# Kernel tuning notes

Measured on AMD Instinct MI355X. Metric: run time of the kernel, lower is better.

The kernel has to match this reference:

```python
import jax, jax.numpy as jnp
import numpy as np

D = 1024
B, T = 4, 2048


def setup_inputs() -> dict:
    key = jax.random.key(0)
    ks = jax.random.split(key, 7)
    s = 0.02
    return {
        "x": jax.random.normal(ks[0], (B, T, D), dtype=jnp.float32),
        "W_in": s * jax.random.normal(ks[1], (2 * D, D), dtype=jnp.float32),
        "b_in": jnp.zeros((2 * D,), dtype=jnp.float32),
        "W_s": s * jax.random.normal(ks[2], (D, D), dtype=jnp.float32),
        "b_s": jnp.zeros((D,), dtype=jnp.float32),
        "W_o": s * jax.random.normal(ks[3], (D, D), dtype=jnp.float32),
        "b_o": jnp.zeros((D,), dtype=jnp.float32),
    }


def _scan_combine(c1, c2):
    # h_t = a_t * h_{t-1} + b_t  -> associative composition of affine maps
    a1, b1 = c1
    a2, b2 = c2
    return a2 * a1, a2 * b1 + b2


def reference(x, W_in, b_in, W_s, b_s, W_o, b_o):
    # Batched projections over all timesteps (h-independent)
    gv = jnp.einsum("btd,ed->bte", x, W_in) + b_in          # [B,T,2D]
    gate = jax.nn.sigmoid(gv[..., :D])                        # [B,T,D]
    val = gv[..., D:]                                         # [B,T,D]
    sv = jnp.tanh(jnp.einsum("btd,ed->bte", val, W_s) + b_s)  # [B,T,D]
    # Linear recurrence h_t = (1-gate_t)*h_{t-1} + gate_t*sv_t, h_0 = 0
    a = 1.0 - gate
    b = gate * sv
    _, h = jax.lax.associative_scan(_scan_combine, (a, b), axis=1)  # h: [B,T,D]
    out = jnp.einsum("btd,ed->bte", h, W_o) + b_o
    return x + out
```

## Files before the change

### kernel.cpp

```cpp
#include <hip/hip_runtime.h>
#include <hip/hip_bf16.h>
#include <cmath>

#define B_DIM 4
#define T_DIM 2048
#define D_DIM 1024
#define M_DIM 8192
#define KP    2048

#define NCH   64
#define CHL   32

using bf16 = __hip_bfloat16;
typedef __attribute__((ext_vector_type(8))) short frag8;
typedef __attribute__((ext_vector_type(4))) float f32x4;

#define XS_OFF   0L
#define WIN_OFF  33554432L
#define WSS_OFF  37748736L
#define WOS_OFF  39845888L
#define GATE_OFF 41943040L
#define VS_OFF   75497472L
#define AF_OFF   92274688L
#define BF_OFF   125829120L
#define ACH_OFF  159383552L
#define BCH_OFF  160432128L

__global__ void split_kernel(const float* __restrict__ src, bf16* __restrict__ dst, long total4) {
    long i4 = (long)blockIdx.x * blockDim.x + threadIdx.x;
    if (i4 >= total4) return;
    long i = i4 * 4;
    const float4 v = *(const float4*)&src[i];
    long r = i >> 10;
    int  c = (int)(i & 1023);
    ushort hi[4], lo[4];
    const float vv[4] = {v.x, v.y, v.z, v.w};
#pragma unroll
    for (int j = 0; j < 4; ++j) {
        bf16 h = __float2bfloat16(vv[j]);
        hi[j] = *(ushort*)&h;
        bf16 l2 = __float2bfloat16(vv[j] - __bfloat162float(h));
        lo[j] = *(ushort*)&l2;
    }
    *(ushort4*)&dst[r * KP + c]        = make_ushort4(hi[0], hi[1], hi[2], hi[3]);
    *(ushort4*)&dst[r * KP + c + 1024] = make_ushort4(lo[0], lo[1], lo[2], lo[3]);
}

__global__ void wconv_kernel(const float* __restrict__ Win, const float* __restrict__ Wsm,
                             const float* __restrict__ Wo,
                             bf16* __restrict__ Wins, bf16* __restrict__ Wss,
                             bf16* __restrict__ Wos) {
    long i4 = (long)blockIdx.x * 256 + threadIdx.x;
    const float* src; bf16* dst; long off;
    if (i4 < 524288)      { src = Win; dst = Wins; off = i4; }
    else if (i4 < 786432) { src = Wsm; dst = Wss;  off = i4 - 524288; }
    else                  { src = Wo;  dst = Wos;  off = i4 - 786432; }
    long i = off * 4;
    const float4 v = *(const float4*)&src[i];
    bf16 h0 = __float2bfloat16(v.x), h1 = __float2bfloat16(v.y);
    bf16 h2 = __float2bfloat16(v.z), h3 = __float2bfloat16(v.w);
    *(ushort4*)&dst[i] = make_ushort4(*(ushort*)&h0, *(ushort*)&h1, *(ushort*)&h2, *(ushort*)&h3);
}

#define AS1 const __attribute__((address_space(1))) void*
#define AS3 __attribute__((address_space(3))) void*

template<int EPI, int NTT, int LDA>
__global__ __launch_bounds__(256, 3)
void gemm128(const bf16* __restrict__ A, const bf16* __restrict__ Bw,
             const float* __restrict__ bias,
             const float* __restrict__ gatef_in,
             const float* __restrict__ x_in,
             float* __restrict__ out0, float* __restrict__ out1,
             bf16* __restrict__ outv)
{
    __shared__ bf16 As[3][4096];
    __shared__ bf16 Bs[3][4096];
    const int t  = threadIdx.x;
    const int l  = t & 63;
    const int w  = t >> 6;
    const int wr = w >> 1, wc = w & 1;
    const int bm = blockIdx.x;
    const int bn = blockIdx.y;

    f32x4 acc[4][4] = {};

    const int sr  = t >> 2;
    const int sg  = (sr & 3) ^ ((sr >> 2) & 3);
    const int scS = ((t & 3) * 8) ^ (sg << 3);
    const bf16* Ab = A  + ((long)bm * 128 + sr) * LDA  + scS;
    const bf16* Bb = Bw + ((long)bn * 128 + sr) * 1024 + scS;

    const int rk    = (((l >> 4) ^ (l & 3) ^ ((l >> 2) & 3)) << 3);
    const int rowA0 = wr * 64 + (l & 15);
    const int rowB0 = wc * 64 + (l & 15);

#define STAGE(slot, kt) {                                                          \
    const long ka = (long)(kt) * 32;                                               \
    const long kb = (long)((kt) & 31) * 32;                                        \
    __builtin_amdgcn_global_load_lds((AS1)(Ab + ka),             (AS3)&As[slot][t * 8],        16, 0, 0); \
    __builtin_amdgcn_global_load_lds((AS1)(Ab + 64 * LDA + ka),  (AS3)&As[slot][2048 + t * 8], 16, 0, 0); \
    __builtin_amdgcn_global_load_lds((AS1)(Bb + kb),             (AS3)&Bs[slot][t * 8],        16, 0, 0); \
    __builtin_amdgcn_global_load_lds((AS1)(Bb + 64 * 1024 + kb), (AS3)&Bs[slot][2048 + t * 8], 16, 0, 0); \
}

    STAGE(0, 0); STAGE(1, 1);
    asm volatile("s_waitcnt vmcnt(4)" ::: "memory");
    __builtin_amdgcn_s_barrier();
    asm volatile("" ::: "memory");

    int sR = 0, sS = 2;
    for (int kt = 0; kt < NTT; ++kt) {
        frag8 fb0 = *(const frag8*)&Bs[sR][(rowB0     ) * 32 + rk];
        frag8 fb1 = *(const frag8*)&Bs[sR][(rowB0 + 16) * 32 + rk];
        frag8 fb2 = *(const frag8*)&Bs[sR][(rowB0 + 32) * 32 + rk];
        frag8 fb3 = *(const frag8*)&Bs[sR][(rowB0 + 48) * 32 + rk];
        frag8 fa0 = *(const frag8*)&As[sR][(rowA0     ) * 32 + rk];
        frag8 fa1 = *(const frag8*)&As[sR][(rowA0 + 16) * 32 + rk];
        frag8 fa2 = *(const frag8*)&As[sR][(rowA0 + 32) * 32 + rk];
        frag8 fa3 = *(const frag8*)&As[sR][(rowA0 + 48) * 32 + rk];
        if (kt + 2 < NTT) STAGE(sS, kt + 2);
        __builtin_amdgcn_s_setprio(1);
        acc[0][0] = __builtin_amdgcn_mfma_f32_16x16x32_bf16(fa0, fb0, acc[0][0], 0, 0, 0);
        acc[0][1] = __builtin_amdgcn_mfma_f32_16x16x32_bf16(fa0, fb1, acc[0][1], 0, 0, 0);
        acc[0][2] = __builtin_amdgcn_mfma_f32_16x16x32_bf16(fa0, fb2, acc[0][2], 0, 0, 0);
        acc[0][3] = __builtin_amdgcn_mfma_f32_16x16x32_bf16(fa0, fb3, acc[0][3], 0, 0, 0);
        acc[1][0] = __builtin_amdgcn_mfma_f32_16x16x32_bf16(fa1, fb0, acc[1][0], 0, 0, 0);
        acc[1][1] = __builtin_amdgcn_mfma_f32_16x16x32_bf16(fa1, fb1, acc[1][1], 0, 0, 0);
        acc[1][2] = __builtin_amdgcn_mfma_f32_16x16x32_bf16(fa1, fb2, acc[1][2], 0, 0, 0);
        acc[1][3] = __builtin_amdgcn_mfma_f32_16x16x32_bf16(fa1, fb3, acc[1][3], 0, 0, 0);
        acc[2][0] = __builtin_amdgcn_mfma_f32_16x16x32_bf16(fa2, fb0, acc[2][0], 0, 0, 0);
        acc[2][1] = __builtin_amdgcn_mfma_f32_16x16x32_bf16(fa2, fb1, acc[2][1], 0, 0, 0);
        acc[2][2] = __builtin_amdgcn_mfma_f32_16x16x32_bf16(fa2, fb2, acc[2][2], 0, 0, 0);
        acc[2][3] = __builtin_amdgcn_mfma_f32_16x16x32_bf16(fa2, fb3, acc[2][3], 0, 0, 0);
        acc[3][0] = __builtin_amdgcn_mfma_f32_16x16x32_bf16(fa3, fb0, acc[3][0], 0, 0, 0);
        acc[3][1] = __builtin_amdgcn_mfma_f32_16x16x32_bf16(fa3, fb1, acc[3][1], 0, 0, 0);
        acc[3][2] = __builtin_amdgcn_mfma_f32_16x16x32_bf16(fa3, fb2, acc[3][2], 0, 0, 0);
        acc[3][3] = __builtin_amdgcn_mfma_f32_16x16x32_bf16(fa3, fb3, acc[3][3], 0, 0, 0);
        __builtin_amdgcn_s_setprio(0);
        asm volatile("" ::: "memory");
        if (kt < NTT - 2)       { asm volatile("s_waitcnt vmcnt(4)" ::: "memory"); }
        else if (kt == NTT - 2) { asm volatile("s_waitcnt vmcnt(0)" ::: "memory"); }
        __builtin_amdgcn_s_barrier();
        asm volatile("" ::: "memory");
        sR = (sR == 2) ? 0 : sR + 1;
        sS = (sS == 2) ? 0 : sS + 1;
    }
#undef STAGE

    const int r4 = (l >> 4) * 4;
    const int cl = l & 15;
#pragma unroll
    for (int fm = 0; fm < 4; ++fm) {
#pragma unroll
        for (int fn = 0; fn < 4; ++fn) {
            const int n = bn * 128 + wc * 64 + fn * 16 + cl;
            const float bn_bias = bias[n];
#pragma unroll
            for (int j = 0; j < 4; ++j) {
                const int m = bm * 128 + wr * 64 + fm * 16 + r4 + j;
                float v = acc[fm][fn][j] + bn_bias;
                if (EPI == 1) {
                    if (n < 1024) {
                        out0[(long)m * 1024 + n] = 1.0f / (1.0f + expf(-v));
                    } else {
                        outv[(long)m * 1024 + (n - 1024)] = __float2bfloat16(v);
                    }
                } else if (EPI == 2) {
                    const float sv = tanhf(v);
                    const float g  = gatef_in[(long)m * 1024 + n];
                    out0[(long)m * 1024 + n] = 1.0f - g;
                    out1[(long)m * 1024 + n] = g * sv;
                } else {
                    out0[(long)m * 1024 + n] = x_in[(long)m * 1024 + n] + v;
                }
            }
        }
    }
}

__global__ void scan_phase1(const float* __restrict__ af, const float* __restrict__ bfv,
                            float* __restrict__ Ach, float* __restrict__ Bch) {
    int tid = blockIdx.x * 256 + threadIdx.x;
    int c = tid >> 12;
    int r = tid & 4095;
    int bi = r >> 10;
    long base = ((long)bi * T_DIM + c * CHL) * D_DIM + (r & 1023);
    float A = 1.0f, Bc = 0.0f;
#pragma unroll 4
    for (int i = 0; i < CHL; ++i) {
        float a = af[base + (long)i * D_DIM];
        float b = bfv[base + (long)i * D_DIM];
        A *= a;
        Bc = a * Bc + b;
    }
    Ach[tid] = A;
    Bch[tid] = Bc;
}

__global__ void scan_phase23(const float* __restrict__ af, const float* __restrict__ bfv,
                             const float* __restrict__ Ach, const float* __restrict__ Bch,
                             bf16* __restrict__ Hs) {
    int tid = blockIdx.x * 256 + threadIdx.x;
    int c = tid >> 12;
    int r = tid & 4095;
    int bi = r >> 10;
    int d  = r & 1023;
    float h = 0.0f;
    for (int j = 0; j < c; ++j)
        h = Ach[j * 4096 + r] * h + Bch[j * 4096 + r];
    long base = ((long)bi * T_DIM + c * CHL) * D_DIM + d;
#pragma unroll 4
    for (int i = 0; i < CHL; ++i) {
        float a = af[base + (long)i * D_DIM];
        float b = bfv[base + (long)i * D_DIM];
        h = a * h + b;
        long m = (long)bi * T_DIM + c * CHL + i;
        Hs[m * 1024 + d] = __float2bfloat16(h);
    }
}

extern "C" void kernel_launch(void* const* d_in, const int* in_sizes, int n_in,
                              void* d_out, int out_size, void* d_ws, size_t ws_size,
                              hipStream_t stream) {
    const float* x   = (const float*)d_in[0];
    const float* Win = (const float*)d_in[1];
    const float* bin = (const float*)d_in[2];
    const float* Wsm = (const float*)d_in[3];
    const float* bs  = (const float*)d_in[4];
    const float* Wo  = (const float*)d_in[5];
    const float* bo  = (const float*)d_in[6];
    float* out = (float*)d_out;
    char*  ws  = (char*)d_ws;

    bf16*  Xs    = (bf16*)(ws + XS_OFF);
    bf16*  Wins  = (bf16*)(ws + WIN_OFF);
    bf16*  Wss   = (bf16*)(ws + WSS_OFF);
    bf16*  Wos   = (bf16*)(ws + WOS_OFF);
    float* gatef = (float*)(ws + GATE_OFF);
    bf16*  Vs    = (bf16*)(ws + VS_OFF);
    float* af    = (float*)(ws + AF_OFF);
    float* bfv   = (float*)(ws + BF_OFF);
    float* Ach   = (float*)(ws + ACH_OFF);
    float* Bch   = (float*)(ws + BCH_OFF);
    bf16*  Hs    = (bf16*)(ws + XS_OFF);

    split_kernel<<<(M_DIM * D_DIM / 4 + 255) / 256, 256, 0, stream>>>(x, Xs, (long)M_DIM * D_DIM / 4);
    wconv_kernel<<<4096, 256, 0, stream>>>(Win, Wsm, Wo, Wins, Wss, Wos);

    dim3 g1(M_DIM / 128, 2048 / 128);
    gemm128<1, 64, 2048><<<g1, 256, 0, stream>>>(Xs, Wins, bin, nullptr, nullptr, gatef, nullptr, Vs);

    dim3 g2(M_DIM / 128, 1024 / 128);
    gemm128<2, 32, 1024><<<g2, 256, 0, stream>>>(Vs, Wss, bs, gatef, nullptr, af, bfv, nullptr);

    scan_phase1 <<<NCH * 4096 / 256, 256, 0, stream>>>(af, bfv, Ach, Bch);
    scan_phase23<<<NCH * 4096 / 256, 256, 0, stream>>>(af, bfv, Ach, Bch, Hs);

    gemm128<3, 32, 1024><<<g2, 256, 0, stream>>>(Hs, Wos, bo, nullptr, x, out, nullptr, nullptr);
}
```

Baseline: 302.2 us.

## Deepen GEMM LDS pipeline to four stages with register double-buffered fragments

Moves the bf16 GEMM main loop from a 3-slot LDS ring to a 4-slot ring with three tiles prefetched. The loop is unrolled by two and ping-pongs two register fragment sets, so the LDS reads for the next tile are issued before the MFMAs on the current one. The aim is to hide global-load and LDS latency behind MFMA work. In exchange, launch bounds drop to 2 blocks per CU, shared memory per block grows to 64 KB, and the fragment registers roughly double, which lowers occupancy.

After: 321.0 us. +6.2%, slower.

```diff
diff --git a/kernel.cpp b/kernel.cpp
--- a/kernel.cpp
+++ b/kernel.cpp
@@ -66,7 +66,7 @@
 #define AS3 __attribute__((address_space(3))) void*
 
 template<int EPI, int NTT, int LDA>
-__global__ __launch_bounds__(256, 3)
+__global__ __launch_bounds__(256, 2)
 void gemm128(const bf16* __restrict__ A, const bf16* __restrict__ Bw,
              const float* __restrict__ bias,
              const float* __restrict__ gatef_in,
@@ -74,8 +74,8 @@
              float* __restrict__ out0, float* __restrict__ out1,
              bf16* __restrict__ outv)
 {
-    __shared__ bf16 As[3][4096];
-    __shared__ bf16 Bs[3][4096];
+    __shared__ bf16 As[4][4096];
+    __shared__ bf16 Bs[4][4096];
     const int t  = threadIdx.x;
     const int l  = t & 63;
     const int w  = t >> 6;
@@ -104,49 +104,77 @@
     __builtin_amdgcn_global_load_lds((AS1)(Bb + 64 * 1024 + kb), (AS3)&Bs[slot][2048 + t * 8], 16, 0, 0); \
 }
 
-    STAGE(0, 0); STAGE(1, 1);
+#define READAB(a0,a1,a2,a3,b0,b1,b2,b3, s) {                                       \
+    b0 = *(const frag8*)&Bs[s][(rowB0     ) * 32 + rk];                            \
+    b1 = *(const frag8*)&Bs[s][(rowB0 + 16) * 32 + rk];                            \
+    b2 = *(const frag8*)&Bs[s][(rowB0 + 32) * 32 + rk];                            \
+    b3 = *(const frag8*)&Bs[s][(rowB0 + 48) * 32 + rk];                            \
+    a0 = *(const frag8*)&As[s][(rowA0     ) * 32 + rk];                            \
+    a1 = *(const frag8*)&As[s][(rowA0 + 16) * 32 + rk];                            \
+    a2 = *(const frag8*)&As[s][(rowA0 + 32) * 32 + rk];                            \
+    a3 = *(const frag8*)&As[s][(rowA0 + 48) * 32 + rk];                            \
+}
+
+#define MFMA16(a0,a1,a2,a3,b0,b1,b2,b3) {                                          \
+    acc[0][0] = __builtin_amdgcn_mfma_f32_16x16x32_bf16(a0, b0, acc[0][0], 0, 0, 0); \
+    acc[0][1] = __builtin_amdgcn_mfma_f32_16x16x32_bf16(a0, b1, acc[0][1], 0, 0, 0); \
+    acc[0][2] = __builtin_amdgcn_mfma_f32_16x16x32_bf16(a0, b2, acc[0][2], 0, 0, 0); \
+    acc[0][3] = __builtin_amdgcn_mfma_f32_16x16x32_bf16(a0, b3, acc[0][3], 0, 0, 0); \
+    acc[1][0] = __builtin_amdgcn_mfma_f32_16x16x32_bf16(a1, b0, acc[1][0], 0, 0, 0); \
+    acc[1][1] = __builtin_amdgcn_mfma_f32_16x16x32_bf16(a1, b1, acc[1][1], 0, 0, 0); \
+    acc[1][2] = __builtin_amdgcn_mfma_f32_16x16x32_bf16(a1, b2, acc[1][2], 0, 0, 0); \
+    acc[1][3] = __builtin_amdgcn_mfma_f32_16x16x32_bf16(a1, b3, acc[1][3], 0, 0, 0); \
+    acc[2][0] = __builtin_amdgcn_mfma_f32_16x16x32_bf16(a2, b0, acc[2][0], 0, 0, 0); \
+    acc[2][1] = __builtin_amdgcn_mfma_f32_16x16x32_bf16(a2, b1, acc[2][1], 0, 0, 0); \
+    acc[2][2] = __builtin_amdgcn_mfma_f32_16x16x32_bf16(a2, b2, acc[2][2], 0, 0, 0); \
+    acc[2][3] = __builtin_amdgcn_mfma_f32_16x16x32_bf16(a2, b3, acc[2][3], 0, 0, 0); \
+    acc[3][0] = __builtin_amdgcn_mfma_f32_16x16x32_bf16(a3, b0, acc[3][0], 0, 0, 0); \
+    acc[3][1] = __builtin_amdgcn_mfma_f32_16x16x32_bf16(a3, b1, acc[3][1], 0, 0, 0); \
+    acc[3][2] = __builtin_amdgcn_mfma_f32_16x16x32_bf16(a3, b2, acc[3][2], 0, 0, 0); \
+    acc[3][3] = __builtin_amdgcn_mfma_f32_16x16x32_bf16(a3, b3, acc[3][3], 0, 0, 0); \
+}
+
+    STAGE(0, 0); STAGE(1, 1); STAGE(2, 2);
     asm volatile("s_waitcnt vmcnt(4)" ::: "memory");
     __builtin_amdgcn_s_barrier();
     asm volatile("" ::: "memory");
 
-    int sR = 0, sS = 2;
-    for (int kt = 0; kt < NTT; ++kt) {
-        frag8 fb0 = *(const frag8*)&Bs[sR][(rowB0     ) * 32 + rk];
-        frag8 fb1 = *(const frag8*)&Bs[sR][(rowB0 + 16) * 32 + rk];
-        frag8 fb2 = *(const frag8*)&Bs[sR][(rowB0 + 32) * 32 + rk];
-        frag8 fb3 = *(const frag8*)&Bs[sR][(rowB0 + 48) * 32 + rk];
-        frag8 fa0 = *(const frag8*)&As[sR][(rowA0     ) * 32 + rk];
-        frag8 fa1 = *(const frag8*)&As[sR][(rowA0 + 16) * 32 + rk];
-        frag8 fa2 = *(const frag8*)&As[sR][(rowA0 + 32) * 32 + rk];
-        frag8 fa3 = *(const frag8*)&As[sR][(rowA0 + 48) * 32 + rk];
-        if (kt + 2 < NTT) STAGE(sS, kt + 2);
+    frag8 xa0, xa1, xa2, xa3, xb0, xb1, xb2, xb3;
+    frag8 ya0, ya1, ya2, ya3, yb0, yb1, yb2, yb3;
+    READAB(xa0, xa1, xa2, xa3, xb0, xb1, xb2, xb3, 0);
+
+#pragma unroll 1
+    for (int kt = 0; kt < NTT; kt += 2) {
+        if (kt + 3 < NTT) STAGE((kt + 3) & 3, kt + 3);
+        READAB(ya0, ya1, ya2, ya3, yb0, yb1, yb2, yb3, (kt + 1) & 3);
         __builtin_amdgcn_s_setprio(1);
-        acc[0][0] = __builtin_amdgcn_mfma_f32_16x16x32_bf16(fa0, fb0, acc[0][0], 0, 0, 0);
-        acc[0][1] = __builtin_amdgcn_mfma_f32_16x16x32_bf16(fa0, fb1, acc[0][1], 0, 0, 0);
-        acc[0][2] = __builtin_amdgcn_mfma_f32_16x16x32_bf16(fa0, fb2, acc[0][2], 0, 0, 0);
-        acc[0][3] = __builtin_amdgcn_mfma_f32_16x16x32_bf16(fa0, fb3, acc[0][3], 0, 0, 0);
-        acc[1][0] = __builtin_amdgcn_mfma_f32_16x16x32_bf16(fa1, fb0, acc[1][0], 0, 0, 0);
-        acc[1][1] = __builtin_amdgcn_mfma_f32_16x16x32_bf16(fa1, fb1, acc[1][1], 0, 0, 0);
-        acc[1][2] = __builtin_amdgcn_mfma_f32_16x16x32_bf16(fa1, fb2, acc[1][2], 0, 0, 0);
-        acc[1][3] = __builtin_amdgcn_mfma_f32_16x16x32_bf16(fa1, fb3, acc[1][3], 0, 0, 0);
-        acc[2][0] = __builtin_amdgcn_mfma_f32_16x16x32_bf16(fa2, fb0, acc[2][0], 0, 0, 0);
-        acc[2][1] = __builtin_amdgcn_mfma_f32_16x16x32_bf16(fa2, fb1, acc[2][1], 0, 0, 0);
-        acc[2][2] = __builtin_amdgcn_mfma_f32_16x16x32_bf16(fa2, fb2, acc[2][2], 0, 0, 0);
-        acc[2][3] = __builtin_amdgcn_mfma_f32_16x16x32_bf16(fa2, fb3, acc[2][3], 0, 0, 0);
-        acc[3][0] = __builtin_amdgcn_mfma_f32_16x16x32_bf16(fa3, fb0, acc[3][0], 0, 0, 0);
-        acc[3][1] = __builtin_amdgcn_mfma_f32_16x16x32_bf16(fa3, fb1, acc[3][1], 0, 0, 0);
-        acc[3][2] = __builtin_amdgcn_mfma_f32_16x16x32_bf16(fa3, fb2, acc[3][2], 0, 0, 0);
-        acc[3][3] = __builtin_amdgcn_mfma_f32_16x16x32_bf16(fa3, fb3, acc[3][3], 0, 0, 0);
+        MFMA16(xa0, xa1, xa2, xa3, xb0, xb1, xb2, xb3);
         __builtin_amdgcn_s_setprio(0);
         asm volatile("" ::: "memory");
-        if (kt < NTT - 2)       { asm volatile("s_waitcnt vmcnt(4)" ::: "memory"); }
-        else if (kt == NTT - 2) { asm volatile("s_waitcnt vmcnt(0)" ::: "memory"); }
-        __builtin_amdgcn_s_barrier();
+        if (kt + 3 < NTT) {
+            asm volatile("s_waitcnt vmcnt(4)" ::: "memory");
+            __builtin_amdgcn_s_barrier();
+            asm volatile("" ::: "memory");
+        }
+        if (kt + 4 < NTT) STAGE(kt & 3, kt + 4);
+        if (kt + 2 < NTT) READAB(xa0, xa1, xa2, xa3, xb0, xb1, xb2, xb3, (kt + 2) & 3);
+        __builtin_amdgcn_s_setprio(1);
+        MFMA16(ya0, ya1, ya2, ya3, yb0, yb1, yb2, yb3);
+        __builtin_amdgcn_s_setprio(0);
         asm volatile("" ::: "memory");
-        sR = (sR == 2) ? 0 : sR + 1;
-        sS = (sS == 2) ? 0 : sS + 1;
+        if (kt + 4 < NTT) {
+            asm volatile("s_waitcnt vmcnt(4)" ::: "memory");
+            __builtin_amdgcn_s_barrier();
+            asm volatile("" ::: "memory");
+        } else if (kt + 2 < NTT) {
+            asm volatile("s_waitcnt vmcnt(0)" ::: "memory");
+            __builtin_amdgcn_s_barrier();
+            asm volatile("" ::: "memory");
+        }
     }
 #undef STAGE
+#undef READAB
+#undef MFMA16
 
     const int r4 = (l >> 4) * 4;
     const int cl = l & 15;
```
